# Kernel tuning notes

Hardware: AMD Instinct MI355X
Metric: run time of the kernel (lower is better)

Reference implementation:

```python
import jax, jax.numpy as jnp
import numpy as np

N_STATES = 25
N_CHANNELS = 80
BATCH = 64
TIME = 400


def setup_inputs() -> dict:
    key = jax.random.key(0)
    k1, k2, k3 = jax.random.split(key, 3)
    alpha_t = jax.random.uniform(k1, (BATCH, TIME, N_STATES), dtype=jnp.float32)
    mu = jax.random.normal(k2, (N_STATES, N_CHANNELS), dtype=jnp.float32)
    D = jax.random.normal(k3, (N_STATES, N_CHANNELS, N_CHANNELS), dtype=jnp.float32)
    # Keras initializer: Constant(log(e - 1)) so softplus(alpha_scaling) == 1 at init
    alpha_scaling = jnp.full((N_STATES,), np.log(np.e - 1.0), dtype=jnp.float32)
    return {"alpha_t": alpha_t, "mu": mu, "D": D, "alpha_scaling": alpha_scaling}


def reference(alpha_t, mu, D, alpha_scaling):
    # a: [batch, time, n_states], scaled per-state by softplus(alpha_scaling)
    a = alpha_t * jax.nn.softplus(alpha_scaling)
    # m_t = sum_j a_jt mu_j  -> [batch, time, channels]
    m_t = jnp.einsum("btj,jc->btc", a, mu)
    # C_t = sum_j a_jt D_j   -> [batch, time, channels, channels]
    C_t = jnp.einsum("btj,jcd->btcd", a, D)
    return (m_t, C_t)
```

## Files before the change

### kernel.cpp

```cpp
#include <hip/hip_runtime.h>
#include <math.h>

#define BATCH 64
#define TIME 400
#define BT (BATCH * TIME)
#define S 25
#define CH 80
#define CD (CH * CH)

#define NTHREADS 256
#define CD_TILE (2 * NTHREADS)
#define ROWS 64

__global__ void scale_kernel(const float* __restrict__ alpha_scaling,
                             float* __restrict__ scale) {
    int k = threadIdx.x;
    if (k < S) {
        float x = alpha_scaling[k];
        scale[k] = fmaxf(x, 0.0f) + log1pf(expf(-fabsf(x)));
    }
}

__global__ __launch_bounds__(NTHREADS) void m_kernel(
    const float* __restrict__ alpha, const float* __restrict__ mu,
    const float* __restrict__ scale, float* __restrict__ out_m) {
    __shared__ float s_mu[S * CH];
    __shared__ float s_scale[S];
    for (int i = threadIdx.x; i < S * CH; i += NTHREADS) s_mu[i] = mu[i];
    if (threadIdx.x < S) s_scale[threadIdx.x] = scale[threadIdx.x];
    __syncthreads();

    int i4 = blockIdx.x * NTHREADS + threadIdx.x;
    const int total4 = BT * CH / 4;
    if (i4 >= total4) return;
    int e = i4 * 4;
    int bt = e / CH;
    int c = e - bt * CH;
    const float* arow = alpha + (size_t)bt * S;
    float4 acc = {0.f, 0.f, 0.f, 0.f};
#pragma unroll
    for (int k = 0; k < S; k++) {
        float a = arow[k] * s_scale[k];
        float4 m4 = *(const float4*)&s_mu[k * CH + c];
        acc.x += a * m4.x;
        acc.y += a * m4.y;
        acc.z += a * m4.z;
        acc.w += a * m4.w;
    }
    *(float4*)&out_m[e] = acc;
}

__global__ __launch_bounds__(NTHREADS) void c_kernel(
    const float* __restrict__ alpha, const float* __restrict__ D,
    const float* __restrict__ scale, float* __restrict__ out_c) {
    const int cd0 = blockIdx.x * CD_TILE;
    const int bt0 = blockIdx.y * ROWS;
    const int vcols = min(CD_TILE, CD - cd0);
    const int c0 = 2 * (int)threadIdx.x;
    if (c0 >= vcols) return;

    float d0[S], d1[S];
#pragma unroll
    for (int k = 0; k < S; ++k) {
        float sc = scale[k];
        float2 dv = *(const float2*)&D[(size_t)k * CD + cd0 + c0];
        d0[k] = dv.x * sc;
        d1[k] = dv.y * sc;
    }

    const float* arow = alpha + (size_t)bt0 * S;
    float* crow = out_c + (size_t)bt0 * CD + cd0 + c0;
    for (int r = 0; r < ROWS; ++r) {
        float acc0 = 0.f, acc1 = 0.f;
#pragma unroll
        for (int k = 0; k < S; ++k) {
            float a = arow[k];
            acc0 = fmaf(a, d0[k], acc0);
            acc1 = fmaf(a, d1[k], acc1);
        }
        float2 v = {acc0, acc1};
        *(float2*)crow = v;
        arow += S;
        crow += CD;
    }
}

extern "C" void kernel_launch(void* const* d_in, const int* in_sizes, int n_in,
                              void* d_out, int out_size, void* d_ws, size_t ws_size,
                              hipStream_t stream) {
    const float* alpha = (const float*)d_in[0];
    const float* mu = (const float*)d_in[1];
    const float* D = (const float*)d_in[2];
    const float* alpha_scaling = (const float*)d_in[3];

    float* out = (float*)d_out;
    float* out_m = out;
    float* out_c = out + BT * CH;
    float* scale = (float*)d_ws;

    scale_kernel<<<1, 64, 0, stream>>>(alpha_scaling, scale);

    const int total4 = BT * CH / 4;
    m_kernel<<<(total4 + NTHREADS - 1) / NTHREADS, NTHREADS, 0, stream>>>(
        alpha, mu, scale, out_m);

    dim3 grid((CD + CD_TILE - 1) / CD_TILE, BT / ROWS);
    c_kernel<<<grid, NTHREADS, 0, stream>>>(alpha, D, scale, out_c);
}
```

Baseline: 721.3 us.

## Widen C kernel to float4 columns, prefetch alpha rows, use nontemporal stores

The C_t kernel now gives each thread 4 output columns, using 320 threads so that 6400 divides into 5 tiles of 1280 exactly, which drops the tail branch. Each thread loads the next row of alpha while computing the current one, and stores results with 128-bit nontemporal writes. The m kernel uses the same vector type and nontemporal stores. The aim is to make the write-bound 655 MB output stream more efficient, at the cost of more registers per thread (100 for D plus 50 for alpha).

```diff
diff --git a/kernel.cpp b/kernel.cpp
--- a/kernel.cpp
+++ b/kernel.cpp
@@ -9,8 +9,13 @@
 #define CD (CH * CH)
 
 #define NTHREADS 256
-#define CD_TILE (2 * NTHREADS)
+
+#define C_THREADS 320
+#define CPT 4
+#define CD_TILE (C_THREADS * CPT)
 #define ROWS 64
+
+typedef float v4f __attribute__((ext_vector_type(4)));
 
 __global__ void scale_kernel(const float* __restrict__ alpha_scaling,
                              float* __restrict__ scale) {
@@ -37,51 +42,56 @@
     int bt = e / CH;
     int c = e - bt * CH;
     const float* arow = alpha + (size_t)bt * S;
-    float4 acc = {0.f, 0.f, 0.f, 0.f};
+    v4f acc = {0.f, 0.f, 0.f, 0.f};
 #pragma unroll
     for (int k = 0; k < S; k++) {
         float a = arow[k] * s_scale[k];
-        float4 m4 = *(const float4*)&s_mu[k * CH + c];
-        acc.x += a * m4.x;
-        acc.y += a * m4.y;
-        acc.z += a * m4.z;
-        acc.w += a * m4.w;
+        v4f m4 = *(const v4f*)&s_mu[k * CH + c];
+        acc += a * m4;
     }
-    *(float4*)&out_m[e] = acc;
+    __builtin_nontemporal_store(acc, (v4f*)&out_m[e]);
 }
 
-__global__ __launch_bounds__(NTHREADS) void c_kernel(
+__global__ __launch_bounds__(C_THREADS) void c_kernel(
     const float* __restrict__ alpha, const float* __restrict__ D,
     const float* __restrict__ scale, float* __restrict__ out_c) {
     const int cd0 = blockIdx.x * CD_TILE;
     const int bt0 = blockIdx.y * ROWS;
-    const int vcols = min(CD_TILE, CD - cd0);
-    const int c0 = 2 * (int)threadIdx.x;
-    if (c0 >= vcols) return;
+    const int c0 = cd0 + CPT * (int)threadIdx.x;
 
-    float d0[S], d1[S];
+    v4f d[S];
 #pragma unroll
     for (int k = 0; k < S; ++k) {
         float sc = scale[k];
-        float2 dv = *(const float2*)&D[(size_t)k * CD + cd0 + c0];
-        d0[k] = dv.x * sc;
-        d1[k] = dv.y * sc;
+        v4f dv = *(const v4f*)&D[(size_t)k * CD + c0];
+        d[k] = dv * sc;
     }
 
     const float* arow = alpha + (size_t)bt0 * S;
-    float* crow = out_c + (size_t)bt0 * CD + cd0 + c0;
-    for (int r = 0; r < ROWS; ++r) {
-        float acc0 = 0.f, acc1 = 0.f;
+    float* crow = out_c + (size_t)bt0 * CD + c0;
+
+    float a_cur[S], a_nxt[S];
 #pragma unroll
-        for (int k = 0; k < S; ++k) {
-            float a = arow[k];
-            acc0 = fmaf(a, d0[k], acc0);
-            acc1 = fmaf(a, d1[k], acc1);
-        }
-        float2 v = {acc0, acc1};
-        *(float2*)crow = v;
+    for (int k = 0; k < S; ++k) a_cur[k] = arow[k];
+
+    for (int r = 0; r < ROWS - 1; ++r) {
+        const float* anext = arow + S;
+#pragma unroll
+        for (int k = 0; k < S; ++k) a_nxt[k] = anext[k];
+        v4f acc = {0.f, 0.f, 0.f, 0.f};
+#pragma unroll
+        for (int k = 0; k < S; ++k) acc = a_cur[k] * d[k] + acc;
+        __builtin_nontemporal_store(acc, (v4f*)crow);
+#pragma unroll
+        for (int k = 0; k < S; ++k) a_cur[k] = a_nxt[k];
         arow += S;
         crow += CD;
+    }
+    {
+        v4f acc = {0.f, 0.f, 0.f, 0.f};
+#pragma unroll
+        for (int k = 0; k < S; ++k) acc = a_cur[k] * d[k] + acc;
+        __builtin_nontemporal_store(acc, (v4f*)crow);
     }
 }
 
@@ -104,6 +114,6 @@
     m_kernel<<<(total4 + NTHREADS - 1) / NTHREADS, NTHREADS, 0, stream>>>(
         alpha, mu, scale, out_m);
 
-    dim3 grid((CD + CD_TILE - 1) / CD_TILE, BT / ROWS);
-    c_kernel<<<grid, NTHREADS, 0, stream>>>(alpha, D, scale, out_c);
+    dim3 grid(CD / CD_TILE, BT / ROWS);
+    c_kernel<<<grid, C_THREADS, 0, stream>>>(alpha, D, scale, out_c);
 }
```

Result: no change. 726.2 us (+0.7%).
